# Kernel tuning notes

Hardware: AMD Instinct MI355X
Metric: run time of the kernel (lower is better)

## Reference

```python
import jax, jax.numpy as jnp
import numpy as np

M, K, L, OUT = 16, 64, 6, 128
IN_CH = 2 + 1 + 1 + 1 + 4 * L  # 29
HID_IN = 128 * 2 + 4           # 260


def setup_inputs() -> dict:
    key = jax.random.key(0)
    ks = jax.random.split(key, 5)
    N = 2_000_000
    P = jax.random.normal(ks[0], (N, 2), jnp.float32) * 2.0
    def lin(k, i, o):
        return jax.random.normal(k, (i, o), jnp.float32) / np.float32(np.sqrt(i))
    return {
        'P': P,
        'W1': lin(ks[1], IN_CH, 64), 'b1': jnp.zeros((64,), jnp.float32),
        'W2': lin(ks[2], 64, 128),   'b2': jnp.zeros((128,), jnp.float32),
        'W3': lin(ks[3], HID_IN, 128), 'b3': jnp.zeros((128,), jnp.float32),
        'W4': lin(ks[4], 128, OUT),  'b4': jnp.zeros((OUT,), jnp.float32),
    }


def _fps(P, m):
    # furthest point sampling, seeded at index 0 (standard convention)
    N = P.shape[0]
    def step(carry, _):
        min_d, last_idx = carry
        last = P[last_idx]
        d = jnp.sum((P - last) ** 2, axis=-1)          # [N]
        min_d = jnp.minimum(min_d, d)
        nxt = jnp.argmax(min_d)
        return (min_d, nxt), last_idx
    init = (jnp.full((N,), jnp.finfo(jnp.float32).max, jnp.float32), jnp.int32(0))
    (_, _), idxs = jax.lax.scan(step, init, None, length=m)
    return idxs  # [m] int


def _gelu(x):
    return jax.nn.gelu(x, approximate=False)  # torch nn.GELU default = erf


def reference(P, W1, b1, W2, b2, W3, b3, W4, b4):
    c_idx = jax.lax.stop_gradient(_fps(P, M))
    C = P[c_idx]                                       # [M,2]
    # brute-force kNN: expanded squared distance avoids [M,N,2] intermediate
    Ps = jax.lax.stop_gradient(P)
    Cs = jax.lax.stop_gradient(C)
    d2 = (jnp.sum(Ps ** 2, -1)[None, :]
          - 2.0 * Cs @ Ps.T
          + jnp.sum(Cs ** 2, -1)[:, None])             # [M,N]
    _, nidx = jax.lax.top_k(-d2, K)                    # [M,K]
    patch = P[nidx]                                    # [M,K,2]
    delta = patch - C[:, None, :]                      # [M,K,2]
    r = jnp.linalg.norm(delta, axis=-1, keepdims=True) # [M,K,1]
    theta = jnp.arctan2(delta[..., 1:2], delta[..., 0:1])
    freqs = (2.0 ** jnp.arange(L)).astype(jnp.float32) # [L]
    ang = delta[..., None, :] * freqs[:, None]         # [M,K,L,2]
    ff = jnp.concatenate([jnp.sin(ang), jnp.cos(ang)], -1).reshape(M, K, 4 * L)
    per_pt = jnp.concatenate([delta, r, jnp.sin(theta), jnp.cos(theta), ff], -1)  # [M,K,29]
    h = _gelu(per_pt @ W1 + b1)
    h = _gelu(h @ W2 + b2)                             # [M,K,128]
    h_max = h.max(axis=1)
    h_mean = h.mean(axis=1)
    rr = r[..., 0]                                     # [M,K]
    stats = jnp.stack([rr.mean(1), rr.max(1), rr.min(1), rr.std(1, ddof=1)], -1)  # [M,4]
    z = jnp.concatenate([h_max, h_mean, stats], -1)    # [M,260]
    F = _gelu(z @ W3 + b3) @ W4 + b4                   # [M,OUT]
    return F, C
```

## Files before the change

### kernel.cpp

```cpp
#include <hip/hip_runtime.h>
#include <math.h>

#define MCENT 16
#define KNN   64
#define NBINS 512
#define RBINS 256
#define CAP   7936
#define FPSB  1024
#define FPST  256
#define MLPT  1024

__device__ __forceinline__ float gelu_f(float x){
    return 0.5f * x * (1.0f + erff(x * 0.70710678118654752440f));
}

__device__ __forceinline__ void xcd_slice(int NP, int B, int bid, int tpb, int tid,
                                          int* q0, int* s1, int* step){
    int xcd = bid & 7, j = bid >> 3, Bx = B >> 3;
    long long np = NP;
    *q0   = (int)((np * xcd) >> 3) + j*tpb + tid;
    *s1   = (int)((np * (xcd+1)) >> 3);
    *step = Bx * tpb;
}

__global__ __launch_bounds__(FPST) void fps_step(
    const float* __restrict__ P, int N,
    float* __restrict__ min_d,
    unsigned long long* __restrict__ partials,
    int k,
    float* __restrict__ cxy,
    float* __restrict__ outC,
    unsigned int* __restrict__ ghist,
    unsigned int* __restrict__ cnt)
{
    const int lane = threadIdx.x & 63;
    const int wid  = threadIdx.x >> 6;
    __shared__ unsigned long long wred[FPST/64];
    __shared__ int s_cur;

    if (k == 0){
        int gi = blockIdx.x*FPST + threadIdx.x;
        if (gi < MCENT*NBINS) ghist[gi] = 0u;
        if (gi < MCENT) cnt[gi] = 0u;
    }

    int cur = 0;
    if (k > 0){
        unsigned long long pb = 0ULL;
        for (int i = threadIdx.x; i < FPSB; i += FPST){
            unsigned long long v = partials[(k-1)*FPSB + i];
            if (v > pb) pb = v;
        }
#pragma unroll
        for (int off = 32; off > 0; off >>= 1){
            unsigned long long o = __shfl_xor(pb, off, 64);
            if (o > pb) pb = o;
        }
        if (lane == 0) wred[wid] = pb;
        __syncthreads();
        if (threadIdx.x == 0){
            unsigned long long b = wred[0];
#pragma unroll
            for (int w = 1; w < FPST/64; ++w) if (wred[w] > b) b = wred[w];
            s_cur = (int)(0xFFFFFFFFu - (unsigned)(b & 0xFFFFFFFFu));
        }
        __syncthreads();
        cur = s_cur;
    }

    if (blockIdx.x == 0 && threadIdx.x == 0){
        float cx = P[2*cur], cy = P[2*cur+1];
        cxy[2*k] = cx; cxy[2*k+1] = cy;
        outC[2*k] = cx; outC[2*k+1] = cy;
    }

    const float cx = P[2*cur], cy = P[2*cur+1];
    unsigned long long bk = 0ULL;
    const int NP = N >> 1;
    int q0, s1, st;
    xcd_slice(NP, gridDim.x, blockIdx.x, FPST, threadIdx.x, &q0, &s1, &st);
    for (int q = q0; q < s1; q += st){
        float4 p = ((const float4*)P)[q];
        float dx0 = __fsub_rn(p.x, cx), dy0 = __fsub_rn(p.y, cy);
        float d0  = __fadd_rn(__fmul_rn(dx0,dx0), __fmul_rn(dy0,dy0));
        float dx1 = __fsub_rn(p.z, cx), dy1 = __fsub_rn(p.w, cy);
        float d1  = __fadd_rn(__fmul_rn(dx1,dx1), __fmul_rn(dy1,dy1));
        float2 mp;
        if (k == 0){ mp.x = d0; mp.y = d1; }
        else {
            mp = ((const float2*)min_d)[q];
            mp.x = fminf(mp.x, d0); mp.y = fminf(mp.y, d1);
        }
        ((float2*)min_d)[q] = mp;
        int g = 2*q;
        unsigned long long k0 =
            ((unsigned long long)__float_as_uint(mp.x) << 32)
            | (unsigned long long)(0xFFFFFFFFu - (unsigned)g);
        unsigned long long k1 =
            ((unsigned long long)__float_as_uint(mp.y) << 32)
            | (unsigned long long)(0xFFFFFFFFu - (unsigned)(g+1));
        if (k0 > bk) bk = k0;
        if (k1 > bk) bk = k1;
    }
    if ((N & 1) && blockIdx.x == 0 && threadIdx.x == 0){
        int g = N-1;
        float dx = __fsub_rn(P[2*g], cx), dy = __fsub_rn(P[2*g+1], cy);
        float d  = __fadd_rn(__fmul_rn(dx,dx), __fmul_rn(dy,dy));
        float nm = (k == 0) ? d : fminf(min_d[g], d);
        min_d[g] = nm;
        unsigned long long kk =
            ((unsigned long long)__float_as_uint(nm) << 32)
            | (unsigned long long)(0xFFFFFFFFu - (unsigned)g);
        if (kk > bk) bk = kk;
    }
#pragma unroll
    for (int off = 32; off > 0; off >>= 1){
        unsigned long long o = __shfl_xor(bk, off, 64);
        if (o > bk) bk = o;
    }
    if (lane == 0) wred[wid] = bk;
    __syncthreads();
    if (threadIdx.x == 0){
        unsigned long long b = wred[0];
#pragma unroll
        for (int w = 1; w < FPST/64; ++w) if (wred[w] > b) b = wred[w];
        partials[k*FPSB + blockIdx.x] = b;
    }
}

__global__ __launch_bounds__(256) void hist_kernel(
    const float* __restrict__ P, int N,
    const unsigned long long* __restrict__ partials,
    float* __restrict__ cxy,
    float* __restrict__ outC,
    unsigned int* __restrict__ ghist,
    unsigned int* __restrict__ rhist)
{
    __shared__ unsigned int h[MCENT*NBINS];
    __shared__ float scx[MCENT], scy[MCENT], scs2[MCENT];
    __shared__ unsigned long long wred[4];
    __shared__ int s_cur;

    {
        unsigned long long pb = 0ULL;
        for (int i = threadIdx.x; i < FPSB; i += 256){
            unsigned long long v = partials[14*FPSB + i];
            if (v > pb) pb = v;
        }
#pragma unroll
        for (int off = 32; off > 0; off >>= 1){
            unsigned long long o = __shfl_xor(pb, off, 64);
            if (o > pb) pb = o;
        }
        if ((threadIdx.x & 63) == 0) wred[threadIdx.x >> 6] = pb;
        __syncthreads();
        if (threadIdx.x == 0){
            unsigned long long b = wred[0];
#pragma unroll
            for (int w = 1; w < 4; ++w) if (wred[w] > b) b = wred[w];
            s_cur = (int)(0xFFFFFFFFu - (unsigned)(b & 0xFFFFFFFFu));
        }
        __syncthreads();
    }
    const int cur15 = s_cur;
    const float c15x = P[2*cur15], c15y = P[2*cur15+1];
    if (blockIdx.x == 0 && threadIdx.x == 0){
        cxy[30] = c15x; cxy[31] = c15y;
        outC[30] = c15x; outC[31] = c15y;
    }

    {
        int gi = blockIdx.x*blockDim.x + threadIdx.x;
        if (gi < MCENT*RBINS) rhist[gi] = 0u;
    }
    for (int i = threadIdx.x; i < MCENT*NBINS; i += blockDim.x) h[i] = 0u;
    if (threadIdx.x < MCENT){
        float a, b;
        if (threadIdx.x == 15){ a = c15x; b = c15y; }
        else { a = cxy[2*threadIdx.x]; b = cxy[2*threadIdx.x+1]; }
        scx[threadIdx.x] = a; scy[threadIdx.x] = b;
        scs2[threadIdx.x] = __fadd_rn(__fmul_rn(a,a), __fmul_rn(b,b));
    }
    __syncthreads();
    const int T    = gridDim.x * blockDim.x;
    const int NP16 = (N >> 1) >> 4;
    for (int q = blockIdx.x*blockDim.x + threadIdx.x; q < NP16; q += T){
        float4 p = ((const float4*)P)[(size_t)q << 4];
        float ps20 = __fadd_rn(__fmul_rn(p.x,p.x), __fmul_rn(p.y,p.y));
        float ps21 = __fadd_rn(__fmul_rn(p.z,p.z), __fmul_rn(p.w,p.w));
#pragma unroll
        for (int m = 0; m < MCENT; ++m){
            float dot0 = __fadd_rn(__fmul_rn(scx[m],p.x), __fmul_rn(scy[m],p.y));
            float d20  = __fadd_rn(__fsub_rn(ps20, __fmul_rn(2.0f,dot0)), scs2[m]);
            atomicAdd(&h[m*NBINS + (__float_as_uint(fmaxf(d20,0.0f)) >> 22)], 1u);
            float dot1 = __fadd_rn(__fmul_rn(scx[m],p.z), __fmul_rn(scy[m],p.w));
            float d21  = __fadd_rn(__fsub_rn(ps21, __fmul_rn(2.0f,dot1)), scs2[m]);
            atomicAdd(&h[m*NBINS + (__float_as_uint(fmaxf(d21,0.0f)) >> 22)], 1u);
        }
    }
    __syncthreads();
    for (int i = threadIdx.x; i < MCENT*NBINS; i += blockDim.x){
        unsigned v = h[i];
        if (v) atomicAdd(&ghist[i], v);
    }
}

__global__ void thr_kernel(const unsigned int* __restrict__ ghist,
                           float* __restrict__ thr,
                           float* __restrict__ sc2){
    int m = threadIdx.x;
    if (m < MCENT){
        unsigned cum = 0; int B = NBINS-1;
        for (int b = 0; b < NBINS; ++b){
            cum += ghist[m*NBINS + b];
            if (cum >= KNN){ B = b; break; }
        }
        float t = __uint_as_float((unsigned)(B+1) << 22);
        thr[m] = t;
        sc2[m] = 255.0f / t;
    }
}

__global__ __launch_bounds__(256) void refine_kernel(
    const float* __restrict__ P, int N,
    const float* __restrict__ cxy,
    const float* __restrict__ sc2,
    unsigned int* __restrict__ rhist)
{
    __shared__ unsigned int h[MCENT*RBINS];
    __shared__ float scx[MCENT], scy[MCENT], scs2[MCENT], ssc[MCENT];
    for (int i = threadIdx.x; i < MCENT*RBINS; i += blockDim.x) h[i] = 0u;
    if (threadIdx.x < MCENT){
        float a = cxy[2*threadIdx.x], b = cxy[2*threadIdx.x+1];
        scx[threadIdx.x]=a; scy[threadIdx.x]=b;
        scs2[threadIdx.x]=__fadd_rn(__fmul_rn(a,a),__fmul_rn(b,b));
        ssc[threadIdx.x]=sc2[threadIdx.x];
    }
    __syncthreads();
    const int NP = N >> 1;
    int q0, s1, st;
    xcd_slice(NP, gridDim.x, blockIdx.x, 256, threadIdx.x, &q0, &s1, &st);
    for (int q = q0; q < s1; q += st){
        float4 p = ((const float4*)P)[q];
        float ps20 = __fadd_rn(__fmul_rn(p.x,p.x), __fmul_rn(p.y,p.y));
        float ps21 = __fadd_rn(__fmul_rn(p.z,p.z), __fmul_rn(p.w,p.w));
#pragma unroll
        for (int m = 0; m < MCENT; ++m){
            float dot0 = __fadd_rn(__fmul_rn(scx[m],p.x), __fmul_rn(scy[m],p.y));
            float d20  = __fadd_rn(__fsub_rn(ps20, __fmul_rn(2.0f,dot0)), scs2[m]);
            int b0 = (int)(fmaxf(d20, 0.0f) * ssc[m]);
            if (b0 < RBINS) atomicAdd(&h[m*RBINS + b0], 1u);
            float dot1 = __fadd_rn(__fmul_rn(scx[m],p.z), __fmul_rn(scy[m],p.w));
            float d21  = __fadd_rn(__fsub_rn(ps21, __fmul_rn(2.0f,dot1)), scs2[m]);
            int b1 = (int)(fmaxf(d21, 0.0f) * ssc[m]);
            if (b1 < RBINS) atomicAdd(&h[m*RBINS + b1], 1u);
        }
    }
    if ((N & 1) && blockIdx.x == 0 && threadIdx.x == 0){
        int g = N-1;
        float x = P[2*g], y = P[2*g+1];
        float ps2 = __fadd_rn(__fmul_rn(x,x), __fmul_rn(y,y));
        for (int m = 0; m < MCENT; ++m){
            float dot = __fadd_rn(__fmul_rn(scx[m],x), __fmul_rn(scy[m],y));
            float d2  = __fadd_rn(__fsub_rn(ps2, __fmul_rn(2.0f,dot)), scs2[m]);
            int b = (int)(fmaxf(d2, 0.0f) * ssc[m]);
            if (b < RBINS) atomicAdd(&h[m*RBINS + b], 1u);
        }
    }
    __syncthreads();
    for (int i = threadIdx.x; i < MCENT*RBINS; i += blockDim.x){
        unsigned v = h[i];
        if (v) atomicAdd(&rhist[i], v);
    }
}

__global__ void thr2_kernel(const unsigned int* __restrict__ rhist,
                            int* __restrict__ B2){
    int m = threadIdx.x;
    if (m < MCENT){
        unsigned cum = 0; int B = RBINS-1;
        for (int b = 0; b < RBINS; ++b){
            cum += rhist[m*RBINS + b];
            if (cum >= KNN){ B = b; break; }
        }
        B2[m] = B;
    }
}

__global__ __launch_bounds__(256) void collect_kernel(
    const float* __restrict__ P, int N,
    const float* __restrict__ cxy,
    const float* __restrict__ sc2,
    const int* __restrict__ B2,
    unsigned int* __restrict__ cnt,
    float* __restrict__ cd2,
    int* __restrict__ cidx)
{
    __shared__ float scx[MCENT], scy[MCENT], scs2[MCENT], ssc[MCENT];
    __shared__ int sB2[MCENT];
    if (threadIdx.x < MCENT){
        float a = cxy[2*threadIdx.x], b = cxy[2*threadIdx.x+1];
        scx[threadIdx.x]=a; scy[threadIdx.x]=b;
        scs2[threadIdx.x]=__fadd_rn(__fmul_rn(a,a),__fmul_rn(b,b));
        ssc[threadIdx.x]=sc2[threadIdx.x];
        sB2[threadIdx.x]=B2[threadIdx.x];
    }
    __syncthreads();
    const int NP = N >> 1;
    int q0, s1, st;
    xcd_slice(NP, gridDim.x, blockIdx.x, 256, threadIdx.x, &q0, &s1, &st);
    for (int q = q0; q < s1; q += st){
        float4 p = ((const float4*)P)[q];
        float ps20 = __fadd_rn(__fmul_rn(p.x,p.x), __fmul_rn(p.y,p.y));
        float ps21 = __fadd_rn(__fmul_rn(p.z,p.z), __fmul_rn(p.w,p.w));
        int g = 2*q;
#pragma unroll
        for (int m = 0; m < MCENT; ++m){
            float dot0 = __fadd_rn(__fmul_rn(scx[m],p.x), __fmul_rn(scy[m],p.y));
            float d20  = __fadd_rn(__fsub_rn(ps20, __fmul_rn(2.0f,dot0)), scs2[m]);
            if ((int)(fmaxf(d20,0.0f) * ssc[m]) <= sB2[m]){
                unsigned pos = atomicAdd(&cnt[m], 1u);
                if (pos < CAP){ cd2[m*CAP+pos]=d20; cidx[m*CAP+pos]=g; }
            }
            float dot1 = __fadd_rn(__fmul_rn(scx[m],p.z), __fmul_rn(scy[m],p.w));
            float d21  = __fadd_rn(__fsub_rn(ps21, __fmul_rn(2.0f,dot1)), scs2[m]);
            if ((int)(fmaxf(d21,0.0f) * ssc[m]) <= sB2[m]){
                unsigned pos = atomicAdd(&cnt[m], 1u);
                if (pos < CAP){ cd2[m*CAP+pos]=d21; cidx[m*CAP+pos]=g+1; }
            }
        }
    }
    if ((N & 1) && blockIdx.x == 0 && threadIdx.x == 0){
        int g = N-1;
        float x = P[2*g], y = P[2*g+1];
        float ps2 = __fadd_rn(__fmul_rn(x,x), __fmul_rn(y,y));
        for (int m = 0; m < MCENT; ++m){
            float dot = __fadd_rn(__fmul_rn(scx[m],x), __fmul_rn(scy[m],y));
            float d2  = __fadd_rn(__fsub_rn(ps2, __fmul_rn(2.0f,dot)), scs2[m]);
            if ((int)(fmaxf(d2,0.0f) * ssc[m]) <= sB2[m]){
                unsigned pos = atomicAdd(&cnt[m], 1u);
                if (pos < CAP){ cd2[m*CAP+pos]=d2; cidx[m*CAP+pos]=g; }
            }
        }
    }
}

__global__ __launch_bounds__(256) void select_kernel(
    const unsigned int* __restrict__ cnt,
    const float* __restrict__ cd2,
    const int* __restrict__ cidx,
    int* __restrict__ nbr)
{
    const int m = blockIdx.x;
    __shared__ unsigned long long keys[CAP];
    unsigned c = cnt[m]; if (c > CAP) c = CAP;
    for (int i = threadIdx.x; i < (int)c; i += 256){
        unsigned u = __float_as_uint(cd2[m*CAP+i]);
        u = (u & 0x80000000u) ? ~u : (u | 0x80000000u);
        keys[i] = ((unsigned long long)u << 32)
                | (unsigned long long)(unsigned)cidx[m*CAP+i];
    }
    __syncthreads();
    for (int i = threadIdx.x; i < (int)c; i += 256){
        unsigned long long ki = keys[i];
        int rank = 0;
        for (int j = 0; j < (int)c; ++j) rank += (keys[j] < ki);
        if (rank < KNN) nbr[m*KNN + rank] = (int)(unsigned)(ki & 0xFFFFFFFFu);
    }
}

__global__ __launch_bounds__(MLPT) void mlp_kernel(
    const float* __restrict__ P,
    const float* __restrict__ cxy,
    const int* __restrict__ nbr,
    const float* __restrict__ W1, const float* __restrict__ b1,
    const float* __restrict__ W2, const float* __restrict__ b2,
    const float* __restrict__ W3, const float* __restrict__ b3,
    const float* __restrict__ W4, const float* __restrict__ b4,
    float* __restrict__ outF)
{
    const int m = blockIdx.x;
    const int tid = threadIdx.x;
    __shared__ float feat[KNN][32];
    __shared__ float h1s[KNN][64];
    __shared__ float sW1[29*64];
    __shared__ float sW2[64*128];
    __shared__ float pmax[8][128], psum[8][128];
    __shared__ float z[260];
    __shared__ float part[8][128];
    __shared__ float zz[128];

    {
        const float4* s2 = (const float4*)W2;
        float4* d2 = (float4*)sW2;
        d2[tid]        = s2[tid];
        d2[tid + 1024] = s2[tid + 1024];
        if (tid < 464) ((float4*)sW1)[tid] = ((const float4*)W1)[tid];
    }

    const float cx = cxy[2*m], cy = cxy[2*m+1];
    if (tid < KNN){
        int g = nbr[m*KNN + tid];
        float dx = P[2*g]   - cx;
        float dy = P[2*g+1] - cy;
        float r  = sqrtf(dx*dx + dy*dy);
        float th = atan2f(dy, dx);
        feat[tid][0]=dx; feat[tid][1]=dy; feat[tid][2]=r;
        feat[tid][3]=sinf(th); feat[tid][4]=cosf(th);
        float fx = dx, fy = dy;
#pragma unroll
        for (int l = 0; l < 6; ++l){
            feat[tid][5+4*l+0]=sinf(fx);
            feat[tid][5+4*l+1]=sinf(fy);
            feat[tid][5+4*l+2]=cosf(fx);
            feat[tid][5+4*l+3]=cosf(fy);
            fx += fx; fy += fy;
        }
    }
    __syncthreads();

#pragma unroll
    for (int rep = 0; rep < 4; ++rep){
        int o = rep*MLPT + tid;
        int k = o >> 6, j = o & 63;
        float acc = b1[j];
#pragma unroll
        for (int c = 0; c < 29; ++c) acc += feat[k][c] * sW1[c*64 + j];
        h1s[k][j] = gelu_f(acc);
    }
    __syncthreads();

    {
        int j = tid & 127, kh = tid >> 7;
        float lmax = -3.402823466e+38f, lsum = 0.f;
        for (int kk = 0; kk < 8; ++kk){
            int k = kh*8 + kk;
            float acc = b2[j];
#pragma unroll 8
            for (int i = 0; i < 64; ++i) acc += h1s[k][i] * sW2[i*128 + j];
            float v = gelu_f(acc);
            lmax = fmaxf(lmax, v);
            lsum += v;
        }
        pmax[kh][j] = lmax; psum[kh][j] = lsum;
    }
    __syncthreads();
    if (tid < 128){
        float mx = pmax[0][tid], sm = psum[0][tid];
#pragma unroll
        for (int w = 1; w < 8; ++w){ mx = fmaxf(mx, pmax[w][tid]); sm += psum[w][tid]; }
        z[tid]       = mx;
        z[128 + tid] = sm * (1.0f/64.0f);
    }
    if (tid >= 128 && tid < 192){
        int l = tid - 128;
        float r = feat[l][2];
        float s = r, mx = r, mn = r;
        for (int off = 1; off < 64; off <<= 1){
            s  += __shfl_xor(s, off, 64);
            mx  = fmaxf(mx, __shfl_xor(mx, off, 64));
            mn  = fminf(mn, __shfl_xor(mn, off, 64));
        }
        float mean = s * (1.0f/64.0f);
        float dv = (r-mean)*(r-mean);
        for (int off = 1; off < 64; off <<= 1) dv += __shfl_xor(dv, off, 64);
        if (l == 0){
            z[256]=mean; z[257]=mx; z[258]=mn; z[259]=sqrtf(dv*(1.0f/63.0f));
        }
    }
    __syncthreads();

    {
        int j = tid & 127, seg = tid >> 7;
        int i0  = (seg < 4) ? seg*33 : 132 + (seg-4)*32;
        int cntn = (seg < 4) ? 33 : 32;
        float acc = 0.f;
        for (int i = i0; i < i0 + cntn; ++i) acc += z[i]*W3[i*128+j];
        part[seg][j] = acc;
    }
    __syncthreads();
    if (tid < 128){
        float a = part[0][tid];
#pragma unroll
        for (int w = 1; w < 8; ++w) a += part[w][tid];
        zz[tid] = gelu_f(a + b3[tid]);
    }
    __syncthreads();
    {
        int j = tid & 127, seg = tid >> 7;
        float acc = 0.f;
#pragma unroll
        for (int i = seg*16; i < seg*16+16; ++i) acc += zz[i]*W4[i*128+j];
        part[seg][j] = acc;
    }
    __syncthreads();
    if (tid < 128){
        float a = part[0][tid];
#pragma unroll
        for (int w = 1; w < 8; ++w) a += part[w][tid];
        outF[m*128 + tid] = a + b4[tid];
    }
}

extern "C" void kernel_launch(void* const* d_in, const int* in_sizes, int n_in,
                              void* d_out, int out_size, void* d_ws, size_t ws_size,
                              hipStream_t stream)
{
    const float* P  = (const float*)d_in[0];
    const float* W1 = (const float*)d_in[1];
    const float* b1 = (const float*)d_in[2];
    const float* W2 = (const float*)d_in[3];
    const float* b2 = (const float*)d_in[4];
    const float* W3 = (const float*)d_in[5];
    const float* b3 = (const float*)d_in[6];
    const float* W4 = (const float*)d_in[7];
    const float* b4 = (const float*)d_in[8];
    int N = in_sizes[0] / 2;
    float* outF = (float*)d_out;
    float* outC = outF + MCENT*128;
    (void)n_in; (void)out_size; (void)ws_size;

    char* base = (char*)d_ws;
    size_t off = 0;
    auto take = [&](size_t bytes)->char*{
        char* p = base + off;
        off = (off + bytes + 255) & ~(size_t)255;
        return p;
    };
    unsigned long long* partials = (unsigned long long*)take((size_t)MCENT*FPSB*8);
    float* cxy         = (float*)take(MCENT*2*4);
    unsigned int* ghist= (unsigned int*)take(MCENT*NBINS*4);
    unsigned int* rhist= (unsigned int*)take(MCENT*RBINS*4);
    unsigned int* cnt  = (unsigned int*)take(MCENT*4);
    float* thr         = (float*)take(MCENT*4);
    float* sc2         = (float*)take(MCENT*4);
    int*   B2          = (int*)  take(MCENT*4);
    int*   nbr         = (int*)  take(MCENT*KNN*4);
    float* cd2         = (float*)take((size_t)MCENT*CAP*4);
    int*   cidx        = (int*)  take((size_t)MCENT*CAP*4);
    float* min_d       = (float*)take((size_t)N*4);

    for (int k = 0; k < MCENT-1; ++k)
        fps_step<<<FPSB, FPST, 0, stream>>>(P, N, min_d, partials, k, cxy, outC,
                                            ghist, cnt);

    hist_kernel<<<128, 256, 0, stream>>>(P, N, partials, cxy, outC, ghist, rhist);
    thr_kernel<<<1, 64, 0, stream>>>(ghist, thr, sc2);
    refine_kernel<<<256, 256, 0, stream>>>(P, N, cxy, sc2, rhist);
    thr2_kernel<<<1, 64, 0, stream>>>(rhist, B2);
    collect_kernel<<<512, 256, 0, stream>>>(P, N, cxy, sc2, B2, cnt, cd2, cidx);
    select_kernel<<<MCENT, 256, 0, stream>>>(cnt, cd2, cidx, nbr);
    mlp_kernel<<<MCENT, MLPT, 0, stream>>>(P, cxy, nbr, W1,b1,W2,b2,W3,b3,W4,b4, outF);
}
```

Before: 310.4 us.

## Fold threshold and select kernels into consumers, skip unchanged min_d writes

Drops the two single-block threshold kernels. Each refine and collect block now loads the global histograms into shared memory and computes the scale and bin threshold itself. The candidate ranking from select_kernel moves into mlp_kernel, with a shared-memory path when there are at most 1024 candidates, which saves three launches and a global round trip for the neighbour list. The FPS step also writes min_d only when a value actually shrank, cutting store traffic on later iterations. In exchange, every block re-reads 48KB of histograms and repeats the serial prefix scan, and the fallback ranking path for more than 1024 candidates reads from global memory in O(c^2).

After: 308.2 us. About the same (-0.7%).

```diff
diff --git a/kernel.cpp b/kernel.cpp
--- a/kernel.cpp
+++ b/kernel.cpp
@@ -6,6 +6,7 @@
 #define NBINS 512
 #define RBINS 256
 #define CAP   7936
+#define SKEYS 1024
 #define FPSB  1024
 #define FPST  256
 #define MLPT  1024
@@ -85,19 +86,22 @@
         float d0  = __fadd_rn(__fmul_rn(dx0,dx0), __fmul_rn(dy0,dy0));
         float dx1 = __fsub_rn(p.z, cx), dy1 = __fsub_rn(p.w, cy);
         float d1  = __fadd_rn(__fmul_rn(dx1,dx1), __fmul_rn(dy1,dy1));
-        float2 mp;
-        if (k == 0){ mp.x = d0; mp.y = d1; }
-        else {
-            mp = ((const float2*)min_d)[q];
-            mp.x = fminf(mp.x, d0); mp.y = fminf(mp.y, d1);
-        }
-        ((float2*)min_d)[q] = mp;
+        float mx, my;
+        if (k == 0){
+            mx = d0; my = d1;
+            ((float2*)min_d)[q] = make_float2(mx, my);
+        } else {
+            float2 mo = ((const float2*)min_d)[q];
+            mx = fminf(mo.x, d0); my = fminf(mo.y, d1);
+            if (mx != mo.x || my != mo.y)
+                ((float2*)min_d)[q] = make_float2(mx, my);
+        }
         int g = 2*q;
         unsigned long long k0 =
-            ((unsigned long long)__float_as_uint(mp.x) << 32)
+            ((unsigned long long)__float_as_uint(mx) << 32)
             | (unsigned long long)(0xFFFFFFFFu - (unsigned)g);
         unsigned long long k1 =
-            ((unsigned long long)__float_as_uint(mp.y) << 32)
+            ((unsigned long long)__float_as_uint(my) << 32)
             | (unsigned long long)(0xFFFFFFFFu - (unsigned)(g+1));
         if (k0 > bk) bk = k0;
         if (k1 > bk) bk = k1;
@@ -205,37 +209,35 @@
     }
 }
 
-__global__ void thr_kernel(const unsigned int* __restrict__ ghist,
-                           float* __restrict__ thr,
-                           float* __restrict__ sc2){
-    int m = threadIdx.x;
-    if (m < MCENT){
+__device__ __forceinline__ void compute_ssc(const unsigned* gh, int tid, float* ssc){
+    if (tid < MCENT){
         unsigned cum = 0; int B = NBINS-1;
         for (int b = 0; b < NBINS; ++b){
-            cum += ghist[m*NBINS + b];
+            cum += gh[tid*NBINS + b];
             if (cum >= KNN){ B = b; break; }
         }
-        float t = __uint_as_float((unsigned)(B+1) << 22);
-        thr[m] = t;
-        sc2[m] = 255.0f / t;
+        ssc[tid] = 255.0f / __uint_as_float((unsigned)(B+1) << 22);
     }
 }
 
 __global__ __launch_bounds__(256) void refine_kernel(
     const float* __restrict__ P, int N,
     const float* __restrict__ cxy,
-    const float* __restrict__ sc2,
+    const unsigned int* __restrict__ ghist,
     unsigned int* __restrict__ rhist)
 {
+    __shared__ unsigned int gh[MCENT*NBINS];
     __shared__ unsigned int h[MCENT*RBINS];
     __shared__ float scx[MCENT], scy[MCENT], scs2[MCENT], ssc[MCENT];
-    for (int i = threadIdx.x; i < MCENT*RBINS; i += blockDim.x) h[i] = 0u;
+    for (int i = threadIdx.x; i < MCENT*NBINS; i += 256) gh[i] = ghist[i];
+    for (int i = threadIdx.x; i < MCENT*RBINS; i += 256) h[i] = 0u;
     if (threadIdx.x < MCENT){
         float a = cxy[2*threadIdx.x], b = cxy[2*threadIdx.x+1];
         scx[threadIdx.x]=a; scy[threadIdx.x]=b;
         scs2[threadIdx.x]=__fadd_rn(__fmul_rn(a,a),__fmul_rn(b,b));
-        ssc[threadIdx.x]=sc2[threadIdx.x];
-    }
+    }
+    __syncthreads();
+    compute_ssc(gh, threadIdx.x, ssc);
     __syncthreads();
     const int NP = N >> 1;
     int q0, s1, st;
@@ -274,36 +276,35 @@
     }
 }
 
-__global__ void thr2_kernel(const unsigned int* __restrict__ rhist,
-                            int* __restrict__ B2){
-    int m = threadIdx.x;
-    if (m < MCENT){
-        unsigned cum = 0; int B = RBINS-1;
-        for (int b = 0; b < RBINS; ++b){
-            cum += rhist[m*RBINS + b];
-            if (cum >= KNN){ B = b; break; }
-        }
-        B2[m] = B;
-    }
-}
-
 __global__ __launch_bounds__(256) void collect_kernel(
     const float* __restrict__ P, int N,
     const float* __restrict__ cxy,
-    const float* __restrict__ sc2,
-    const int* __restrict__ B2,
+    const unsigned int* __restrict__ ghist,
+    const unsigned int* __restrict__ rhist,
     unsigned int* __restrict__ cnt,
     float* __restrict__ cd2,
     int* __restrict__ cidx)
 {
+    __shared__ unsigned int gh[MCENT*NBINS];
+    __shared__ unsigned int rh[MCENT*RBINS];
     __shared__ float scx[MCENT], scy[MCENT], scs2[MCENT], ssc[MCENT];
     __shared__ int sB2[MCENT];
+    for (int i = threadIdx.x; i < MCENT*NBINS; i += 256) gh[i] = ghist[i];
+    for (int i = threadIdx.x; i < MCENT*RBINS; i += 256) rh[i] = rhist[i];
     if (threadIdx.x < MCENT){
         float a = cxy[2*threadIdx.x], b = cxy[2*threadIdx.x+1];
         scx[threadIdx.x]=a; scy[threadIdx.x]=b;
         scs2[threadIdx.x]=__fadd_rn(__fmul_rn(a,a),__fmul_rn(b,b));
-        ssc[threadIdx.x]=sc2[threadIdx.x];
-        sB2[threadIdx.x]=B2[threadIdx.x];
+    }
+    __syncthreads();
+    compute_ssc(gh, threadIdx.x, ssc);
+    if (threadIdx.x < MCENT){
+        unsigned cum = 0; int B = RBINS-1;
+        for (int b = 0; b < RBINS; ++b){
+            cum += rh[threadIdx.x*RBINS + b];
+            if (cum >= KNN){ B = b; break; }
+        }
+        sB2[threadIdx.x] = B;
     }
     __syncthreads();
     const int NP = N >> 1;
@@ -345,34 +346,12 @@
     }
 }
 
-__global__ __launch_bounds__(256) void select_kernel(
+__global__ __launch_bounds__(MLPT) void mlp_kernel(
+    const float* __restrict__ P,
+    const float* __restrict__ cxy,
     const unsigned int* __restrict__ cnt,
     const float* __restrict__ cd2,
     const int* __restrict__ cidx,
-    int* __restrict__ nbr)
-{
-    const int m = blockIdx.x;
-    __shared__ unsigned long long keys[CAP];
-    unsigned c = cnt[m]; if (c > CAP) c = CAP;
-    for (int i = threadIdx.x; i < (int)c; i += 256){
-        unsigned u = __float_as_uint(cd2[m*CAP+i]);
-        u = (u & 0x80000000u) ? ~u : (u | 0x80000000u);
-        keys[i] = ((unsigned long long)u << 32)
-                | (unsigned long long)(unsigned)cidx[m*CAP+i];
-    }
-    __syncthreads();
-    for (int i = threadIdx.x; i < (int)c; i += 256){
-        unsigned long long ki = keys[i];
-        int rank = 0;
-        for (int j = 0; j < (int)c; ++j) rank += (keys[j] < ki);
-        if (rank < KNN) nbr[m*KNN + rank] = (int)(unsigned)(ki & 0xFFFFFFFFu);
-    }
-}
-
-__global__ __launch_bounds__(MLPT) void mlp_kernel(
-    const float* __restrict__ P,
-    const float* __restrict__ cxy,
-    const int* __restrict__ nbr,
     const float* __restrict__ W1, const float* __restrict__ b1,
     const float* __restrict__ W2, const float* __restrict__ b2,
     const float* __restrict__ W3, const float* __restrict__ b3,
@@ -389,6 +368,8 @@
     __shared__ float z[260];
     __shared__ float part[8][128];
     __shared__ float zz[128];
+    __shared__ unsigned long long kkeys[SKEYS];
+    __shared__ int snbr[KNN];
 
     {
         const float4* s2 = (const float4*)W2;
@@ -398,9 +379,43 @@
         if (tid < 464) ((float4*)sW1)[tid] = ((const float4*)W1)[tid];
     }
 
+    unsigned c = cnt[m]; if (c > CAP) c = CAP;
+    if (c <= SKEYS){
+        if (tid < (int)c){
+            unsigned u = __float_as_uint(cd2[m*CAP+tid]);
+            u = (u & 0x80000000u) ? ~u : (u | 0x80000000u);
+            kkeys[tid] = ((unsigned long long)u << 32)
+                       | (unsigned long long)(unsigned)cidx[m*CAP+tid];
+        }
+        __syncthreads();
+        if (tid < (int)c){
+            unsigned long long ki = kkeys[tid];
+            int rank = 0;
+            for (int j = 0; j < (int)c; ++j) rank += (kkeys[j] < ki);
+            if (rank < KNN) snbr[rank] = (int)(unsigned)(ki & 0xFFFFFFFFu);
+        }
+    } else {
+        for (int i = tid; i < (int)c; i += MLPT){
+            unsigned ui = __float_as_uint(cd2[m*CAP+i]);
+            ui = (ui & 0x80000000u) ? ~ui : (ui | 0x80000000u);
+            unsigned long long ki = ((unsigned long long)ui << 32)
+                                  | (unsigned long long)(unsigned)cidx[m*CAP+i];
+            int rank = 0;
+            for (int j = 0; j < (int)c; ++j){
+                unsigned uj = __float_as_uint(cd2[m*CAP+j]);
+                uj = (uj & 0x80000000u) ? ~uj : (uj | 0x80000000u);
+                unsigned long long kj = ((unsigned long long)uj << 32)
+                                      | (unsigned long long)(unsigned)cidx[m*CAP+j];
+                rank += (kj < ki);
+            }
+            if (rank < KNN) snbr[rank] = (int)(unsigned)(ki & 0xFFFFFFFFu);
+        }
+    }
+    __syncthreads();
+
     const float cx = cxy[2*m], cy = cxy[2*m+1];
     if (tid < KNN){
-        int g = nbr[m*KNN + tid];
+        int g = snbr[tid];
         float dx = P[2*g]   - cx;
         float dy = P[2*g+1] - cy;
         float r  = sqrtf(dx*dx + dy*dy);
@@ -425,7 +440,7 @@
         int k = o >> 6, j = o & 63;
         float acc = b1[j];
 #pragma unroll
-        for (int c = 0; c < 29; ++c) acc += feat[k][c] * sW1[c*64 + j];
+        for (int cc = 0; cc < 29; ++cc) acc += feat[k][cc] * sW1[cc*64 + j];
         h1s[k][j] = gelu_f(acc);
     }
     __syncthreads();
@@ -532,10 +547,6 @@
     unsigned int* ghist= (unsigned int*)take(MCENT*NBINS*4);
     unsigned int* rhist= (unsigned int*)take(MCENT*RBINS*4);
     unsigned int* cnt  = (unsigned int*)take(MCENT*4);
-    float* thr         = (float*)take(MCENT*4);
-    float* sc2         = (float*)take(MCENT*4);
-    int*   B2          = (int*)  take(MCENT*4);
-    int*   nbr         = (int*)  take(MCENT*KNN*4);
     float* cd2         = (float*)take((size_t)MCENT*CAP*4);
     int*   cidx        = (int*)  take((size_t)MCENT*CAP*4);
     float* min_d       = (float*)take((size_t)N*4);
@@ -545,10 +556,8 @@
                                             ghist, cnt);
 
     hist_kernel<<<128, 256, 0, stream>>>(P, N, partials, cxy, outC, ghist, rhist);
-    thr_kernel<<<1, 64, 0, stream>>>(ghist, thr, sc2);
-    refine_kernel<<<256, 256, 0, stream>>>(P, N, cxy, sc2, rhist);
-    thr2_kernel<<<1, 64, 0, stream>>>(rhist, B2);
-    collect_kernel<<<512, 256, 0, stream>>>(P, N, cxy, sc2, B2, cnt, cd2, cidx);
-    select_kernel<<<MCENT, 256, 0, stream>>>(cnt, cd2, cidx, nbr);
-    mlp_kernel<<<MCENT, MLPT, 0, stream>>>(P, cxy, nbr, W1,b1,W2,b2,W3,b3,W4,b4, outF);
-}
+    refine_kernel<<<256, 256, 0, stream>>>(P, N, cxy, ghist, rhist);
+    collect_kernel<<<512, 256, 0, stream>>>(P, N, cxy, ghist, rhist, cnt, cd2, cidx);
+    mlp_kernel<<<MCENT, MLPT, 0, stream>>>(P, cxy, cnt, cd2, cidx,
+                                           W1,b1,W2,b2,W3,b3,W4,b4, outF);
+}
```
